# Kernel tuning notes

Measured on AMD Instinct MI355X. Metric: run time of the kernel, lower is better.

Reference implementation:

```python
import jax, jax.numpy as jnp
import numpy as np

BS, X_RW, H = 16384, 768, 256  # batch, x + R*W, hidden
D_IN = X_RW + 2 * H            # 1280 = x + R*W + 2*h


def setup_inputs() -> dict:
    key = jax.random.key(0)
    ks = jax.random.split(key, 13)
    scale = 1.0 / np.sqrt(D_IN)  # nn.Linear default init range
    def lin(kw, kb):
        w = jax.random.uniform(kw, (D_IN, H), jnp.float32, -scale, scale)
        b = jax.random.uniform(kb, (H,), jnp.float32, -scale, scale)
        return w, b
    Wi, bi = lin(ks[0], ks[1])
    Wf, bf = lin(ks[2], ks[3])
    Wo, bo = lin(ks[4], ks[5])
    Ws, bs_ = lin(ks[6], ks[7])
    return {
        "input_x": jax.random.normal(ks[8], (BS, X_RW), jnp.float32),
        "previous_time": jax.random.normal(ks[9], (BS, H), jnp.float32),
        "previous_layer": jax.random.normal(ks[10], (BS, H), jnp.float32),
        "old_state": jax.random.normal(ks[11], (BS, H), jnp.float32),
        "Wi": Wi, "bi": bi, "Wf": Wf, "bf": bf,
        "Wo": Wo, "bo": bo, "Ws": Ws, "bs_": bs_,
    }


def reference(input_x, previous_time, previous_layer, old_state,
              Wi, bi, Wf, bf, Wo, bo, Ws, bs_):
    # concat once, fuse the four gate GEMMs into one [D_IN, 4H] GEMM
    s = jnp.concatenate([input_x, previous_time, previous_layer], axis=1)  # [bs, D_IN]
    W4 = jnp.concatenate([Wi, Wf, Wo, Ws], axis=1)   # [D_IN, 4H]
    b4 = jnp.concatenate([bi, bf, bo, bs_], axis=0)  # [4H]
    g = s @ W4 + b4                                   # [bs, 4H]
    i_g, f_g, o_g, c_g = jnp.split(g, 4, axis=1)
    input_gate = jax.nn.sigmoid(i_g)
    forget_gate = jax.nn.sigmoid(f_g)
    output_gate = jax.nn.sigmoid(o_g)
    new_state = forget_gate * old_state + input_gate * jnp.tanh(c_g)
    new_hidden = output_gate * jnp.tanh(new_state)
    return (new_hidden, new_state)
```

## Files before the change

kernel.cpp:

```cpp
#include <hip/hip_runtime.h>
#include <stdint.h>

#define BS   16384
#define XRW  768
#define HD   256
#define DIN  1280
#define N4   1024
#define NKT  20

typedef __attribute__((ext_vector_type(4))) float f32x4;
typedef __attribute__((ext_vector_type(8))) short s16x8;
typedef __attribute__((ext_vector_type(4))) unsigned int u32x4;

__device__ __forceinline__ unsigned short f2bf(float f) {
  uint32_t u = __builtin_bit_cast(uint32_t, f);
  u += 0x7FFFu + ((u >> 16) & 1u);
  return (unsigned short)(u >> 16);
}
__device__ __forceinline__ uint32_t cvtpk(float a, float b) {
  uint32_t d;
  asm("v_cvt_pk_bf16_f32 %0, %1, %2" : "=v"(d) : "v"(a), "v"(b));
  return d;
}
__device__ __forceinline__ float sigmoidf_(float x) {
  return 1.0f / (1.0f + __expf(-x));
}
__device__ __forceinline__ float tanhf_(float x) {
  return 1.0f - 2.0f / (__expf(2.0f * x) + 1.0f);
}
__device__ __forceinline__ void gload16(const void* g, void* l) {
  __builtin_amdgcn_global_load_lds((const __attribute__((address_space(1))) void*)g,
                                   (__attribute__((address_space(3))) void*)l, 16, 0, 0);
}

__global__ void conv_w_kernel(const float* __restrict__ Wi,
                              const float* __restrict__ Wf,
                              const float* __restrict__ Wo,
                              const float* __restrict__ Ws,
                              unsigned short* __restrict__ Wt) {
  const int np = blockIdx.x;
  const int g = (np >> 4) & 3;
  const int h = ((np >> 6) << 4) + (np & 15);
  const float* W = (g == 0) ? Wi : (g == 1) ? Wf : (g == 2) ? Wo : Ws;
  for (int k = threadIdx.x; k < DIN; k += 256)
    Wt[np * DIN + k] = f2bf(W[k * HD + h]);
}

__global__ __launch_bounds__(512, 2)
void lstm_gemm_kernel(const float* __restrict__ X,
                      const float* __restrict__ PT,
                      const float* __restrict__ PL,
                      const unsigned short* __restrict__ Wt,
                      const float* __restrict__ BI,
                      const float* __restrict__ BF,
                      const float* __restrict__ BO,
                      const float* __restrict__ BSv,
                      const float* __restrict__ OLD,
                      float* __restrict__ out) {
  __shared__ unsigned char smem[131072];
  const int tid  = threadIdx.x;
  const int wid  = tid >> 6;
  const int lane = tid & 63;

  const int H = blockIdx.x;
  const int xcd = H & 7, slot = H >> 3;
  const int mt = xcd * 8 + (slot >> 2);
  const int nt = slot & 3;
  const int wr = wid >> 2, wc = wid & 3;

  const int r8   = lane >> 3;
  const int scol = ((lane & 7) ^ r8) << 4;
  const char* gB = (const char*)Wt + (size_t)(nt * 256 + wid * 8 + r8) * (DIN * 2) + scol;

#define STAGE_B(t1, oB) do {                                                  \
    const int kb_ = (t1) * 128;                                               \
    _Pragma("unroll")                                                         \
    for (int c_ = 0; c_ < 4; ++c_)                                            \
      gload16(gB + (size_t)c_ * (64 * DIN * 2) + kb_,                         \
              &smem[65536 + (oB) + c_ * 8192 + wid * 1024]);                  \
  } while (0)

  const int arow  = tid >> 3;
  const int a7    = tid & 7;
  const int awcol = ((a7 ^ (arow & 7)) << 4);

#define ALOAD(t1, h, R0, R1, R2, R3) do {                                     \
    const float* asrc_; int astr_, aoff_;                                     \
    if ((t1) < 12)      { asrc_ = X;  astr_ = XRW; aoff_ = (t1) * 64; }       \
    else if ((t1) < 16) { asrc_ = PT; astr_ = HD;  aoff_ = ((t1) - 12) * 64; }\
    else                { asrc_ = PL; astr_ = HD;  aoff_ = ((t1) - 16) * 64; }\
    const float* ga_ = asrc_ + (size_t)(mt * 256 + arow + (h) * 128) * astr_  \
                             + aoff_ + a7 * 8;                                \
    R0 = *(const f32x4*)(ga_);                                                \
    R1 = *(const f32x4*)(ga_ + 4);                                            \
    R2 = *(const f32x4*)(ga_ + (size_t)64 * astr_);                           \
    R3 = *(const f32x4*)(ga_ + (size_t)64 * astr_ + 4);                       \
  } while (0)

#define AWRITE(oB, h, R0, R1, R2, R3) do {                                    \
    u32x4 w0_, w1_;                                                           \
    w0_.x = cvtpk(R0.x, R0.y); w0_.y = cvtpk(R0.z, R0.w);                     \
    w0_.z = cvtpk(R1.x, R1.y); w0_.w = cvtpk(R1.z, R1.w);                     \
    w1_.x = cvtpk(R2.x, R2.y); w1_.y = cvtpk(R2.z, R2.w);                     \
    w1_.z = cvtpk(R3.x, R3.y); w1_.w = cvtpk(R3.z, R3.w);                     \
    *(u32x4*)(&smem[(oB) + ((arow + (h) * 128)      << 7) + awcol]) = w0_;    \
    *(u32x4*)(&smem[(oB) + ((arow + (h) * 128 + 64) << 7) + awcol]) = w1_;    \
  } while (0)

  const int rx   = lane & 15;
  const int axor = (lane & 7) << 4;
  const int col0 = (((lane >> 4) << 4)) ^ axor;
  const int col1 = (64 + ((lane >> 4) << 4)) ^ axor;
  const int aRow = (wr * 128 + rx) * 128;
  const int bRow = 65536 + (wc * 64 + rx) * 128;

  f32x4 acc[8][4];
  #pragma unroll
  for (int i = 0; i < 8; ++i)
    #pragma unroll
    for (int j = 0; j < 4; ++j) {
      f32x4 z = {0.0f, 0.0f, 0.0f, 0.0f};
      acc[i][j] = z;
    }

#define VMW(N) asm volatile("s_waitcnt vmcnt(" #N ")" ::: "memory")
#define LGKM0() do { asm volatile("s_waitcnt lgkmcnt(0)" ::: "memory");       \
                     __builtin_amdgcn_sched_barrier(0); } while (0)
#define FRAGS(bo_, kh_col) do {                                               \
    _Pragma("unroll")                                                         \
    for (int nf = 0; nf < 4; ++nf)                                            \
      bq[nf] = *(const s16x8*)(&smem[(bo_) + bRow + nf * 2048 + (kh_col)]);   \
    _Pragma("unroll")                                                         \
    for (int mf = 0; mf < 8; ++mf)                                            \
      aq[mf] = *(const s16x8*)(&smem[(bo_) + aRow + mf * 2048 + (kh_col)]);   \
  } while (0)
#define MFMAS() do {                                                          \
    __builtin_amdgcn_s_setprio(1);                                            \
    _Pragma("unroll")                                                         \
    for (int mf = 0; mf < 8; ++mf)                                            \
      _Pragma("unroll")                                                       \
      for (int nf = 0; nf < 4; ++nf)                                          \
        acc[mf][nf] = __builtin_amdgcn_mfma_f32_16x16x32_bf16(aq[mf], bq[nf], \
                                                      acc[mf][nf], 0, 0, 0);  \
    __builtin_amdgcn_s_setprio(0);                                            \
  } while (0)

  {
    f32x4 p0, p1, p2, p3;
    ALOAD(0, 0, p0, p1, p2, p3);
    STAGE_B(0, 0);
    VMW(4);
    AWRITE(0, 0, p0, p1, p2, p3);
    ALOAD(0, 1, p0, p1, p2, p3);
    VMW(0);
    AWRITE(0, 1, p0, p1, p2, p3);
    LGKM0();
    __builtin_amdgcn_s_barrier();
  }

  for (int kt = 0; kt < NKT; ++kt) {
    const int c = kt & 1, o = c ^ 1;
    const int bo_ = c << 15;
    const int oo_ = o << 15;
    const bool pf = (kt + 1) < NKT;
    s16x8 aq[8], bq[4];
    f32x4 ar0, ar1, ar2, ar3;

    if (pf) ALOAD(kt + 1, 0, ar0, ar1, ar2, ar3);
    FRAGS(bo_, col0);
    if (pf) STAGE_B(kt + 1, oo_);
    MFMAS();
    VMW(4);
    if (pf) { AWRITE(oo_, 0, ar0, ar1, ar2, ar3); ALOAD(kt + 1, 1, ar0, ar1, ar2, ar3); }
    FRAGS(bo_, col1);
    MFMAS();
    VMW(0);
    if (pf) AWRITE(oo_, 1, ar0, ar1, ar2, ar3);
    LGKM0();
    __builtin_amdgcn_s_barrier();
  }

  {
    const int hq = nt * 64 + wc * 16 + rx;
    const float bbi = BI[hq], bbf = BF[hq], bbo = BO[hq], bbs = BSv[hq];
    const int m0 = mt * 256 + wr * 128 + (lane >> 4) * 4;
    float* outNS = out + (size_t)BS * HD;
    #pragma unroll
    for (int mf = 0; mf < 8; ++mf) {
      const int mrow = m0 + mf * 16;
      float old_[4];
      #pragma unroll
      for (int r = 0; r < 4; ++r)
        old_[r] = OLD[(size_t)(mrow + r) * HD + hq];
      #pragma unroll
      for (int r = 0; r < 4; ++r) {
        const float ig = sigmoidf_(acc[mf][0][r] + bbi);
        const float fg = sigmoidf_(acc[mf][1][r] + bbf);
        const float og = sigmoidf_(acc[mf][2][r] + bbo);
        const float cg = tanhf_(acc[mf][3][r] + bbs);
        const float ns = fg * old_[r] + ig * cg;
        const float nh = og * tanhf_(ns);
        out[(size_t)(mrow + r) * HD + hq]   = nh;
        outNS[(size_t)(mrow + r) * HD + hq] = ns;
      }
    }
  }
#undef STAGE_B
#undef ALOAD
#undef AWRITE
#undef VMW
#undef LGKM0
#undef FRAGS
#undef MFMAS
}

extern "C" void kernel_launch(void* const* d_in, const int* in_sizes, int n_in,
                              void* d_out, int out_size, void* d_ws, size_t ws_size,
                              hipStream_t stream) {
  const float* X   = (const float*)d_in[0];
  const float* PT  = (const float*)d_in[1];
  const float* PL  = (const float*)d_in[2];
  const float* OLD = (const float*)d_in[3];
  const float* Wi  = (const float*)d_in[4];
  const float* bi  = (const float*)d_in[5];
  const float* Wf  = (const float*)d_in[6];
  const float* bfv = (const float*)d_in[7];
  const float* Wo  = (const float*)d_in[8];
  const float* bo  = (const float*)d_in[9];
  const float* Ws  = (const float*)d_in[10];
  const float* bsv = (const float*)d_in[11];
  float* out = (float*)d_out;

  unsigned short* Wt = (unsigned short*)d_ws;

  conv_w_kernel<<<N4, 256, 0, stream>>>(Wi, Wf, Wo, Ws, Wt);
  lstm_gemm_kernel<<<256, 512, 0, stream>>>(X, PT, PL, Wt, bi, bfv, bo, bsv, OLD, out);
}
```

Measured before the change: 63.08 us.

## Triple-buffer B tiles and split K-step into four barrier-separated MFMA quadrants

Raises LDS to 160KB so B tiles are triple-buffered with a two-step prefetch distance, while A stays double-buffered. Each K-tile is split into four quadrant MFMA groups with interleaved LDS reads, global loads and stores, separated by workgroup barriers. The aim is to hide global-load latency and spread LDS traffic across the MFMA work. The cost is many more barriers per tile and higher LDS use, which on MI355X may limit the kernel to one block per CU despite launch_bounds(512,2).

```diff
diff --git a/kernel.cpp b/kernel.cpp
--- a/kernel.cpp
+++ b/kernel.cpp
@@ -57,7 +57,7 @@
                       const float* __restrict__ BSv,
                       const float* __restrict__ OLD,
                       float* __restrict__ out) {
-  __shared__ unsigned char smem[131072];
+  __shared__ unsigned char smem[163840];
   const int tid  = threadIdx.x;
   const int wid  = tid >> 6;
   const int lane = tid & 63;
@@ -72,12 +72,12 @@
   const int scol = ((lane & 7) ^ r8) << 4;
   const char* gB = (const char*)Wt + (size_t)(nt * 256 + wid * 8 + r8) * (DIN * 2) + scol;
 
-#define STAGE_B(t1, oB) do {                                                  \
+#define STAGE_BH(t1, bb, h) do {                                              \
     const int kb_ = (t1) * 128;                                               \
     _Pragma("unroll")                                                         \
-    for (int c_ = 0; c_ < 4; ++c_)                                            \
+    for (int c_ = 2 * (h); c_ < 2 * (h) + 2; ++c_)                            \
       gload16(gB + (size_t)c_ * (64 * DIN * 2) + kb_,                         \
-              &smem[65536 + (oB) + c_ * 8192 + wid * 1024]);                  \
+              &smem[65536 + (bb) * 32768 + c_ * 8192 + wid * 1024]);          \
   } while (0)
 
   const int arow  = tid >> 3;
@@ -97,14 +97,14 @@
     R3 = *(const f32x4*)(ga_ + (size_t)64 * astr_ + 4);                       \
   } while (0)
 
-#define AWRITE(oB, h, R0, R1, R2, R3) do {                                    \
+#define AWRITE(ab, h, R0, R1, R2, R3) do {                                    \
     u32x4 w0_, w1_;                                                           \
     w0_.x = cvtpk(R0.x, R0.y); w0_.y = cvtpk(R0.z, R0.w);                     \
     w0_.z = cvtpk(R1.x, R1.y); w0_.w = cvtpk(R1.z, R1.w);                     \
     w1_.x = cvtpk(R2.x, R2.y); w1_.y = cvtpk(R2.z, R2.w);                     \
     w1_.z = cvtpk(R3.x, R3.y); w1_.w = cvtpk(R3.z, R3.w);                     \
-    *(u32x4*)(&smem[(oB) + ((arow + (h) * 128)      << 7) + awcol]) = w0_;    \
-    *(u32x4*)(&smem[(oB) + ((arow + (h) * 128 + 64) << 7) + awcol]) = w1_;    \
+    *(u32x4*)(&smem[(ab) * 32768 + ((arow + (h) * 128)      << 7) + awcol]) = w0_; \
+    *(u32x4*)(&smem[(ab) * 32768 + ((arow + (h) * 128 + 64) << 7) + awcol]) = w1_; \
   } while (0)
 
   const int rx   = lane & 15;
@@ -112,7 +112,7 @@
   const int col0 = (((lane >> 4) << 4)) ^ axor;
   const int col1 = (64 + ((lane >> 4) << 4)) ^ axor;
   const int aRow = (wr * 128 + rx) * 128;
-  const int bRow = 65536 + (wc * 64 + rx) * 128;
+  const int bRow = (wc * 64 + rx) * 128;
 
   f32x4 acc[8][4];
   #pragma unroll
@@ -126,59 +126,92 @@
 #define VMW(N) asm volatile("s_waitcnt vmcnt(" #N ")" ::: "memory")
 #define LGKM0() do { asm volatile("s_waitcnt lgkmcnt(0)" ::: "memory");       \
                      __builtin_amdgcn_sched_barrier(0); } while (0)
-#define FRAGS(bo_, kh_col) do {                                               \
-    _Pragma("unroll")                                                         \
-    for (int nf = 0; nf < 4; ++nf)                                            \
-      bq[nf] = *(const s16x8*)(&smem[(bo_) + bRow + nf * 2048 + (kh_col)]);   \
-    _Pragma("unroll")                                                         \
-    for (int mf = 0; mf < 8; ++mf)                                            \
-      aq[mf] = *(const s16x8*)(&smem[(bo_) + aRow + mf * 2048 + (kh_col)]);   \
-  } while (0)
-#define MFMAS() do {                                                          \
+#define RD_A(ab, mh) do {                                                     \
+    _Pragma("unroll")                                                         \
+    for (int mf = 0; mf < 4; ++mf) {                                          \
+      aqh[mf * 2 + 0] = *(const s16x8*)(&smem[(ab) * 32768 + aRow + (mh) * 8192 + mf * 2048 + col0]); \
+      aqh[mf * 2 + 1] = *(const s16x8*)(&smem[(ab) * 32768 + aRow + (mh) * 8192 + mf * 2048 + col1]); \
+    }                                                                         \
+  } while (0)
+#define RD_B(bb, nh, BQ) do {                                                 \
+    _Pragma("unroll")                                                         \
+    for (int nf = 0; nf < 2; ++nf) {                                          \
+      BQ[nf * 2 + 0] = *(const s16x8*)(&smem[65536 + (bb) * 32768 + bRow + (nh) * 4096 + nf * 2048 + col0]); \
+      BQ[nf * 2 + 1] = *(const s16x8*)(&smem[65536 + (bb) * 32768 + bRow + (nh) * 4096 + nf * 2048 + col1]); \
+    }                                                                         \
+  } while (0)
+#define QUAD(mh, nh, BQ) do {                                                 \
     __builtin_amdgcn_s_setprio(1);                                            \
     _Pragma("unroll")                                                         \
-    for (int mf = 0; mf < 8; ++mf)                                            \
+    for (int mf = 0; mf < 4; ++mf)                                            \
       _Pragma("unroll")                                                       \
-      for (int nf = 0; nf < 4; ++nf)                                          \
-        acc[mf][nf] = __builtin_amdgcn_mfma_f32_16x16x32_bf16(aq[mf], bq[nf], \
-                                                      acc[mf][nf], 0, 0, 0);  \
+      for (int nf = 0; nf < 2; ++nf)                                          \
+        _Pragma("unroll")                                                     \
+        for (int kh = 0; kh < 2; ++kh)                                        \
+          acc[(mh) * 4 + mf][(nh) * 2 + nf] =                                 \
+            __builtin_amdgcn_mfma_f32_16x16x32_bf16(aqh[mf * 2 + kh],         \
+                BQ[nf * 2 + kh], acc[(mh) * 4 + mf][(nh) * 2 + nf], 0, 0, 0); \
     __builtin_amdgcn_s_setprio(0);                                            \
   } while (0)
 
+#define TILE4(t1, AB, BB, BW, PFA, PFB) do {                                  \
+    s16x8 aqh[8], bq0[4], bq1[4];                                             \
+    f32x4 ar0, ar1, ar2, ar3, as0, as1, as2, as3;                             \
+                          \
+    if (PFA) ALOAD((t1) + 1, 0, ar0, ar1, ar2, ar3);                          \
+    RD_A(AB, 0);                                                              \
+    RD_B(BB, 0, bq0);                                                         \
+    __builtin_amdgcn_s_barrier();                                             \
+    LGKM0();                                                                  \
+    QUAD(0, 0, bq0);                                                          \
+    __builtin_amdgcn_s_barrier();                                             \
+                                                      \
+    RD_B(BB, 1, bq1);                                                         \
+    __builtin_amdgcn_s_barrier();                                             \
+    LGKM0();                                                                  \
+    QUAD(0, 1, bq1);                                                          \
+    __builtin_amdgcn_s_barrier();                                             \
+         \
+    if (PFB) STAGE_BH((t1) + 2, BW, 0);                                       \
+    if (PFA) { AWRITE((AB) ^ 1, 0, ar0, ar1, ar2, ar3);                       \
+               ALOAD((t1) + 1, 1, as0, as1, as2, as3); }                      \
+    RD_A(AB, 1);                                                              \
+    __builtin_amdgcn_s_barrier();                                             \
+    LGKM0();                                                                  \
+    QUAD(1, 1, bq1);                                                          \
+    __builtin_amdgcn_s_barrier();                                             \
+      \
+                      \
+    if (PFB) STAGE_BH((t1) + 2, BW, 1);                                       \
+    if (PFA) AWRITE((AB) ^ 1, 1, as0, as1, as2, as3);                         \
+    LGKM0();                                                                  \
+    __builtin_amdgcn_s_barrier();                                             \
+    QUAD(1, 0, bq0);                                                          \
+  } while (0)
+
   {
-    f32x4 p0, p1, p2, p3;
+    f32x4 p0, p1, p2, p3, q0, q1, q2, q3;
     ALOAD(0, 0, p0, p1, p2, p3);
-    STAGE_B(0, 0);
+    ALOAD(0, 1, q0, q1, q2, q3);
+    STAGE_BH(0, 0, 0); STAGE_BH(0, 0, 1);
+    STAGE_BH(1, 1, 0); STAGE_BH(1, 1, 1);
+    AWRITE(0, 0, p0, p1, p2, p3);
+    AWRITE(0, 1, q0, q1, q2, q3);
     VMW(4);
-    AWRITE(0, 0, p0, p1, p2, p3);
-    ALOAD(0, 1, p0, p1, p2, p3);
-    VMW(0);
-    AWRITE(0, 1, p0, p1, p2, p3);
     LGKM0();
     __builtin_amdgcn_s_barrier();
   }
 
-  for (int kt = 0; kt < NKT; ++kt) {
-    const int c = kt & 1, o = c ^ 1;
-    const int bo_ = c << 15;
-    const int oo_ = o << 15;
-    const bool pf = (kt + 1) < NKT;
-    s16x8 aq[8], bq[4];
-    f32x4 ar0, ar1, ar2, ar3;
-
-    if (pf) ALOAD(kt + 1, 0, ar0, ar1, ar2, ar3);
-    FRAGS(bo_, col0);
-    if (pf) STAGE_B(kt + 1, oo_);
-    MFMAS();
-    VMW(4);
-    if (pf) { AWRITE(oo_, 0, ar0, ar1, ar2, ar3); ALOAD(kt + 1, 1, ar0, ar1, ar2, ar3); }
-    FRAGS(bo_, col1);
-    MFMAS();
-    VMW(0);
-    if (pf) AWRITE(oo_, 1, ar0, ar1, ar2, ar3);
-    LGKM0();
-    __builtin_amdgcn_s_barrier();
+  for (int j = 0; j < 18; j += 6) {
+    TILE4(j + 0, 0, 0, 2, true, true);
+    TILE4(j + 1, 1, 1, 0, true, true);
+    TILE4(j + 2, 0, 2, 1, true, true);
+    TILE4(j + 3, 1, 0, 2, true, true);
+    TILE4(j + 4, 0, 1, 0, true, true);
+    TILE4(j + 5, 1, 2, 1, true, true);
   }
+  TILE4(18, 0, 0, 2, true, false);
+  TILE4(19, 1, 1, 0, false, false);
 
   {
     const int hq = nt * 64 + wc * 16 + rx;
@@ -205,13 +238,15 @@
       }
     }
   }
-#undef STAGE_B
+#undef STAGE_BH
 #undef ALOAD
 #undef AWRITE
 #undef VMW
 #undef LGKM0
-#undef FRAGS
-#undef MFMAS
+#undef RD_A
+#undef RD_B
+#undef QUAD
+#undef TILE4
 }
 
 extern "C" void kernel_launch(void* const* d_in, const int* in_sizes, int n_in,
```

After: 97.62 us. 1.55x slower.

## Load B fragments directly from global into registers, shrink tile to 128x256

Applied to the files above, without the earlier changes.

Changes the GEMM tiling from 256x256 tiles with 512 threads to 128x256 tiles with 256 threads and 512 blocks. B weight fragments are now loaded straight from global memory into registers and double-buffered there, instead of being staged through LDS with global_load_lds. LDS drops to 32KB, holding only the double-buffered A tile. The aim is to cut LDS traffic and footprint and raise occupancy. In exchange the per-lane B loads are less coalesced, and A reuse across the N dimension is lower, so global traffic for A doubles.

```diff
diff --git a/kernel.cpp b/kernel.cpp
--- a/kernel.cpp
+++ b/kernel.cpp
@@ -27,10 +27,6 @@
 }
 __device__ __forceinline__ float tanhf_(float x) {
   return 1.0f - 2.0f / (__expf(2.0f * x) + 1.0f);
-}
-__device__ __forceinline__ void gload16(const void* g, void* l) {
-  __builtin_amdgcn_global_load_lds((const __attribute__((address_space(1))) void*)g,
-                                   (__attribute__((address_space(3))) void*)l, 16, 0, 0);
 }
 
 __global__ void conv_w_kernel(const float* __restrict__ Wi,
@@ -46,7 +42,7 @@
     Wt[np * DIN + k] = f2bf(W[k * HD + h]);
 }
 
-__global__ __launch_bounds__(512, 2)
+__global__ __launch_bounds__(256, 2)
 void lstm_gemm_kernel(const float* __restrict__ X,
                       const float* __restrict__ PT,
                       const float* __restrict__ PL,
@@ -57,27 +53,28 @@
                       const float* __restrict__ BSv,
                       const float* __restrict__ OLD,
                       float* __restrict__ out) {
-  __shared__ unsigned char smem[131072];
+  __shared__ unsigned char smem[32768];
   const int tid  = threadIdx.x;
   const int wid  = tid >> 6;
   const int lane = tid & 63;
 
   const int H = blockIdx.x;
   const int xcd = H & 7, slot = H >> 3;
-  const int mt = xcd * 8 + (slot >> 2);
-  const int nt = slot & 3;
-  const int wr = wid >> 2, wc = wid & 3;
-
-  const int r8   = lane >> 3;
-  const int scol = ((lane & 7) ^ r8) << 4;
-  const char* gB = (const char*)Wt + (size_t)(nt * 256 + wid * 8 + r8) * (DIN * 2) + scol;
-
-#define STAGE_B(t1, oB) do {                                                  \
-    const int kb_ = (t1) * 128;                                               \
+  const int mt2 = xcd * 16 + (slot >> 2);
+  const int ntB = slot & 3;
+
+  const int rx = lane & 15;
+  const int kg = lane >> 4;
+
+  const char* gBw = (const char*)Wt + (size_t)(ntB * 256 + wid * 64 + rx) * (DIN * 2) + kg * 16;
+
+#define BLOAD(t1, BQ) do {                                                    \
+    const char* gb_ = gBw + (t1) * 128;                                       \
     _Pragma("unroll")                                                         \
-    for (int c_ = 0; c_ < 4; ++c_)                                            \
-      gload16(gB + (size_t)c_ * (64 * DIN * 2) + kb_,                         \
-              &smem[65536 + (oB) + c_ * 8192 + wid * 1024]);                  \
+    for (int nf = 0; nf < 4; ++nf) {                                          \
+      BQ[nf * 2 + 0] = *(const s16x8*)(gb_ + (size_t)nf * (16 * DIN * 2));    \
+      BQ[nf * 2 + 1] = *(const s16x8*)(gb_ + (size_t)nf * (16 * DIN * 2) + 64); \
+    }                                                                         \
   } while (0)
 
   const int arow  = tid >> 3;
@@ -89,30 +86,28 @@
     if ((t1) < 12)      { asrc_ = X;  astr_ = XRW; aoff_ = (t1) * 64; }       \
     else if ((t1) < 16) { asrc_ = PT; astr_ = HD;  aoff_ = ((t1) - 12) * 64; }\
     else                { asrc_ = PL; astr_ = HD;  aoff_ = ((t1) - 16) * 64; }\
-    const float* ga_ = asrc_ + (size_t)(mt * 256 + arow + (h) * 128) * astr_  \
+    const float* ga_ = asrc_ + (size_t)(mt2 * 128 + arow + (h) * 64) * astr_  \
                              + aoff_ + a7 * 8;                                \
     R0 = *(const f32x4*)(ga_);                                                \
     R1 = *(const f32x4*)(ga_ + 4);                                            \
-    R2 = *(const f32x4*)(ga_ + (size_t)64 * astr_);                           \
-    R3 = *(const f32x4*)(ga_ + (size_t)64 * astr_ + 4);                       \
-  } while (0)
-
-#define AWRITE(oB, h, R0, R1, R2, R3) do {                                    \
+    R2 = *(const f32x4*)(ga_ + (size_t)32 * astr_);                           \
+    R3 = *(const f32x4*)(ga_ + (size_t)32 * astr_ + 4);                       \
+  } while (0)
+
+#define AWRITE(ab, h, R0, R1, R2, R3) do {                                    \
     u32x4 w0_, w1_;                                                           \
     w0_.x = cvtpk(R0.x, R0.y); w0_.y = cvtpk(R0.z, R0.w);                     \
     w0_.z = cvtpk(R1.x, R1.y); w0_.w = cvtpk(R1.z, R1.w);                     \
     w1_.x = cvtpk(R2.x, R2.y); w1_.y = cvtpk(R2.z, R2.w);                     \
     w1_.z = cvtpk(R3.x, R3.y); w1_.w = cvtpk(R3.z, R3.w);                     \
-    *(u32x4*)(&smem[(oB) + ((arow + (h) * 128)      << 7) + awcol]) = w0_;    \
-    *(u32x4*)(&smem[(oB) + ((arow + (h) * 128 + 64) << 7) + awcol]) = w1_;    \
-  } while (0)
-
-  const int rx   = lane & 15;
+    *(u32x4*)(&smem[(ab) * 16384 + ((arow + (h) * 64)      << 7) + awcol]) = w0_; \
+    *(u32x4*)(&smem[(ab) * 16384 + ((arow + (h) * 64 + 32) << 7) + awcol]) = w1_; \
+  } while (0)
+
   const int axor = (lane & 7) << 4;
-  const int col0 = (((lane >> 4) << 4)) ^ axor;
+  const int col0 = ((lane >> 4) << 4) ^ axor;
   const int col1 = (64 + ((lane >> 4) << 4)) ^ axor;
-  const int aRow = (wr * 128 + rx) * 128;
-  const int bRow = 65536 + (wc * 64 + rx) * 128;
+  const int aRow = rx * 128;
 
   f32x4 acc[8][4];
   #pragma unroll
@@ -123,67 +118,62 @@
       acc[i][j] = z;
     }
 
-#define VMW(N) asm volatile("s_waitcnt vmcnt(" #N ")" ::: "memory")
 #define LGKM0() do { asm volatile("s_waitcnt lgkmcnt(0)" ::: "memory");       \
                      __builtin_amdgcn_sched_barrier(0); } while (0)
-#define FRAGS(bo_, kh_col) do {                                               \
-    _Pragma("unroll")                                                         \
-    for (int nf = 0; nf < 4; ++nf)                                            \
-      bq[nf] = *(const s16x8*)(&smem[(bo_) + bRow + nf * 2048 + (kh_col)]);   \
+#define RD_A(ab, kcol) do {                                                   \
     _Pragma("unroll")                                                         \
     for (int mf = 0; mf < 8; ++mf)                                            \
-      aq[mf] = *(const s16x8*)(&smem[(bo_) + aRow + mf * 2048 + (kh_col)]);   \
-  } while (0)
-#define MFMAS() do {                                                          \
+      aq[mf] = *(const s16x8*)(&smem[(ab) * 16384 + aRow + mf * 2048 + (kcol)]); \
+  } while (0)
+#define MF16(BQ, kh) do {                                                     \
     __builtin_amdgcn_s_setprio(1);                                            \
     _Pragma("unroll")                                                         \
     for (int mf = 0; mf < 8; ++mf)                                            \
       _Pragma("unroll")                                                       \
       for (int nf = 0; nf < 4; ++nf)                                          \
-        acc[mf][nf] = __builtin_amdgcn_mfma_f32_16x16x32_bf16(aq[mf], bq[nf], \
-                                                      acc[mf][nf], 0, 0, 0);  \
+        acc[mf][nf] = __builtin_amdgcn_mfma_f32_16x16x32_bf16(aq[mf],         \
+                          BQ[nf * 2 + (kh)], acc[mf][nf], 0, 0, 0);           \
     __builtin_amdgcn_s_setprio(0);                                            \
   } while (0)
 
+#define TILE(t1, AB, BC, BN, PF) do {                                         \
+    s16x8 aq[8];                                                              \
+    f32x4 ar0, ar1, ar2, ar3;                                                 \
+    if (PF) ALOAD((t1) + 1, 0, ar0, ar1, ar2, ar3);          \
+    if (PF) BLOAD((t1) + 1, BN);                          \
+    RD_A(AB, col0);                                                           \
+    MF16(BC, 0);                                                              \
+    if (PF) { AWRITE((AB) ^ 1, 0, ar0, ar1, ar2, ar3);                        \
+              ALOAD((t1) + 1, 1, ar0, ar1, ar2, ar3); }                       \
+    RD_A(AB, col1);                                                           \
+    MF16(BC, 1);                                                              \
+    if (PF) AWRITE((AB) ^ 1, 1, ar0, ar1, ar2, ar3);                          \
+    LGKM0();                                                                  \
+    __builtin_amdgcn_s_barrier();                                             \
+  } while (0)
+
+  s16x8 bqA[8], bqB[8];
+
   {
-    f32x4 p0, p1, p2, p3;
+    f32x4 p0, p1, p2, p3, q0, q1, q2, q3;
     ALOAD(0, 0, p0, p1, p2, p3);
-    STAGE_B(0, 0);
-    VMW(4);
+    ALOAD(0, 1, q0, q1, q2, q3);
+    BLOAD(0, bqA);
     AWRITE(0, 0, p0, p1, p2, p3);
-    ALOAD(0, 1, p0, p1, p2, p3);
-    VMW(0);
-    AWRITE(0, 1, p0, p1, p2, p3);
+    AWRITE(0, 1, q0, q1, q2, q3);
     LGKM0();
     __builtin_amdgcn_s_barrier();
   }
 
-  for (int kt = 0; kt < NKT; ++kt) {
-    const int c = kt & 1, o = c ^ 1;
-    const int bo_ = c << 15;
-    const int oo_ = o << 15;
-    const bool pf = (kt + 1) < NKT;
-    s16x8 aq[8], bq[4];
-    f32x4 ar0, ar1, ar2, ar3;
-
-    if (pf) ALOAD(kt + 1, 0, ar0, ar1, ar2, ar3);
-    FRAGS(bo_, col0);
-    if (pf) STAGE_B(kt + 1, oo_);
-    MFMAS();
-    VMW(4);
-    if (pf) { AWRITE(oo_, 0, ar0, ar1, ar2, ar3); ALOAD(kt + 1, 1, ar0, ar1, ar2, ar3); }
-    FRAGS(bo_, col1);
-    MFMAS();
-    VMW(0);
-    if (pf) AWRITE(oo_, 1, ar0, ar1, ar2, ar3);
-    LGKM0();
-    __builtin_amdgcn_s_barrier();
+  for (int j = 0; j < NKT; j += 2) {
+    TILE(j,     0, bqA, bqB, (j + 1) < NKT);
+    TILE(j + 1, 1, bqB, bqA, (j + 2) < NKT);
   }
 
   {
-    const int hq = nt * 64 + wc * 16 + rx;
+    const int hq = (ntB * 4 + wid) * 16 + rx;
     const float bbi = BI[hq], bbf = BF[hq], bbo = BO[hq], bbs = BSv[hq];
-    const int m0 = mt * 256 + wr * 128 + (lane >> 4) * 4;
+    const int m0 = mt2 * 128 + (lane >> 4) * 4;
     float* outNS = out + (size_t)BS * HD;
     #pragma unroll
     for (int mf = 0; mf < 8; ++mf) {
@@ -205,13 +195,13 @@
       }
     }
   }
-#undef STAGE_B
+#undef BLOAD
 #undef ALOAD
 #undef AWRITE
-#undef VMW
 #undef LGKM0
-#undef FRAGS
-#undef MFMAS
+#undef RD_A
+#undef MF16
+#undef TILE
 }
 
 extern "C" void kernel_launch(void* const* d_in, const int* in_sizes, int n_in,
@@ -234,5 +224,5 @@
   unsigned short* Wt = (unsigned short*)d_ws;
 
   conv_w_kernel<<<N4, 256, 0, stream>>>(Wi, Wf, Wo, Ws, Wt);
-  lstm_gemm_kernel<<<256, 512, 0, stream>>>(X, PT, PL, Wt, bi, bfv, bo, bsv, OLD, out);
-}
+  lstm_gemm_kernel<<<512, 256, 0, stream>>>(X, PT, PL, Wt, bi, bfv, bo, bsv, OLD, out);
+}
```

Result: slower. 220.7 us (+249.9%).
